# Kernel optimization log

Hardware: AMD Instinct MI355X
Metric: run time of the kernel (lower is better)

Reference implementation:

```python
import jax, jax.numpy as jnp
import numpy as np

H = 128          # hidden/context/decoder dim
HEADS = 4
HEAD_DIM = H // HEADS
MAX_LENGTH = 64
VOCAB = 3


def _lstm_step(h, c, x, Wih, Whh, b):
    # PyTorch gate order: i, f, g, o
    gates = x @ Wih.T + h @ Whh.T + b
    i, f, g, o = jnp.split(gates, 4, axis=-1)
    c = jax.nn.sigmoid(f) * c + jax.nn.sigmoid(i) * jnp.tanh(g)
    h = jax.nn.sigmoid(o) * jnp.tanh(c)
    return h, c


def _run_lstm(x, Wih, Whh, b):
    # x: (T, B, D) -> (T, B, H); zero initial state (PyTorch default)
    B = x.shape[1]
    Hh = Whh.shape[1]
    init = (jnp.zeros((B, Hh), x.dtype), jnp.zeros((B, Hh), x.dtype))
    def step(carry, xt):
        h, c = carry
        h, c = _lstm_step(h, c, xt, Wih, Whh, b)
        return (h, c), h
    _, ys = jax.lax.scan(step, init, x)
    return ys


def setup_inputs() -> dict:
    key = jax.random.key(0)
    T, B, D = 512, 64, 1024
    ks = jax.random.split(key, 20)
    def p(k, shape, s=0.05):
        return jax.random.normal(k, shape, dtype=jnp.float32) * s
    return {
        "cnn_output": p(ks[0], (T, B, D), 1.0),
        # encoder LSTM (2 layers); biases fused (b_ih + b_hh)
        "enc_Wih0": p(ks[1], (4 * H, D)),
        "enc_Whh0": p(ks[2], (4 * H, H)),
        "enc_b0": p(ks[3], (4 * H,)),
        "enc_Wih1": p(ks[4], (4 * H, H)),
        "enc_Whh1": p(ks[5], (4 * H, H)),
        "enc_b1": p(ks[6], (4 * H,)),
        # MultiheadAttention(embed_dim=128, num_heads=4)
        "attn_in_w": p(ks[7], (3 * H, H)),
        "attn_in_b": p(ks[8], (3 * H,)),
        "attn_out_w": p(ks[9], (H, H)),
        "attn_out_b": p(ks[10], (H,)),
        # decoder LSTM (2 layers), input dim 256
        "dec_Wih0": p(ks[11], (4 * H, 2 * H)),
        "dec_Whh0": p(ks[12], (4 * H, H)),
        "dec_b0": p(ks[13], (4 * H,)),
        "dec_Wih1": p(ks[14], (4 * H, H)),
        "dec_Whh1": p(ks[15], (4 * H, H)),
        "dec_b1": p(ks[16], (4 * H,)),
        # output projection
        "lin_w": p(ks[17], (VOCAB, H)),
        "lin_b": p(ks[18], (VOCAB,)),
    }


def reference(cnn_output, enc_Wih0, enc_Whh0, enc_b0, enc_Wih1, enc_Whh1, enc_b1,
              attn_in_w, attn_in_b, attn_out_w, attn_out_b,
              dec_Wih0, dec_Whh0, dec_b0, dec_Wih1, dec_Whh1, dec_b1,
              lin_w, lin_b):
    T, B, _ = cnn_output.shape
    # ---- encoder: 2-layer LSTM over T ----
    enc = _run_lstm(cnn_output, enc_Wih0, enc_Whh0, enc_b0)
    enc = _run_lstm(enc, enc_Wih1, enc_Whh1, enc_b1)          # (T, B, H)

    # ---- precompute attention keys/values (encoding is fixed) ----
    Wq, Wk, Wv = jnp.split(attn_in_w, 3, axis=0)
    bq, bk, bv = jnp.split(attn_in_b, 3, axis=0)
    K = (enc @ Wk.T + bk).reshape(T, B, HEADS, HEAD_DIM)      # (T,B,h,d)
    V = (enc @ Wv.T + bv).reshape(T, B, HEADS, HEAD_DIM)
    scale = 1.0 / np.sqrt(HEAD_DIM)

    # ---- 64-step attention + 2-layer LSTM decode loop ----
    out0 = jnp.zeros((B, H), cnn_output.dtype)
    h0 = jnp.zeros((2, B, H), cnn_output.dtype)
    c0 = jnp.zeros((2, B, H), cnn_output.dtype)

    def step(carry, _):
        out, h, c = carry
        q = ((out @ Wq.T + bq) * scale).reshape(B, HEADS, HEAD_DIM)
        scores = jnp.einsum("bhd,tbhd->bht", q, K)            # (B,h,T)
        attn = jax.nn.softmax(scores, axis=-1)
        ctx = jnp.einsum("bht,tbhd->bhd", attn, V).reshape(B, H)
        ctx = ctx @ attn_out_w.T + attn_out_b
        x = jnp.concatenate([out, ctx], axis=-1)              # (B, 2H)
        nh0, nc0 = _lstm_step(h[0], c[0], x, dec_Wih0, dec_Whh0, dec_b0)
        nh1, nc1 = _lstm_step(h[1], c[1], nh0, dec_Wih1, dec_Whh1, dec_b1)
        new_out = jax.nn.relu(nh1)
        y = new_out @ lin_w.T + lin_b                          # (B, vocab)
        return (new_out, jnp.stack([nh0, nh1]), jnp.stack([nc0, nc1])), y

    _, ys = jax.lax.scan(step, (out0, h0, c0), None, length=MAX_LENGTH)
    return ys                                                  # (64, B, vocab)
```

## Files before the change

### kernel.cpp

```cpp
#include <hip/hip_runtime.h>
#include <math.h>

#define T_LEN 512
#define BATCH 64
#define HID 128
#define G4 512

#define OFF_WQ2   0
#define OFF_WXO   16384
#define OFF_WXC   81920
#define OFF_WHH0b 147456
#define OFF_WIH1b 212992
#define OFF_WHH1b 278528
#define W2_TOTAL  344064

__device__ __forceinline__ float sigf(float x) { return 1.0f / (1.0f + __expf(-x)); }

__device__ __forceinline__ unsigned short f2bf(float x) {
    unsigned u = __float_as_uint(x);
    unsigned r = (u + 0x7fffu + ((u >> 16) & 1u)) >> 16;
    return (unsigned short)r;
}

__device__ __forceinline__ void cvt8(uint4 u, float f[8]) {
    f[0] = __uint_as_float(u.x << 16); f[1] = __uint_as_float(u.x & 0xffff0000u);
    f[2] = __uint_as_float(u.y << 16); f[3] = __uint_as_float(u.y & 0xffff0000u);
    f[4] = __uint_as_float(u.z << 16); f[5] = __uint_as_float(u.z & 0xffff0000u);
    f[6] = __uint_as_float(u.w << 16); f[7] = __uint_as_float(u.w & 0xffff0000u);
}

#define KEEP4(Vv) asm volatile("" : "+v"((Vv).x), "+v"((Vv).y), "+v"((Vv).z), "+v"((Vv).w))

__device__ __forceinline__ void cstore(float* p, float v) {
    __hip_atomic_store(p, v, __ATOMIC_RELAXED, __HIP_MEMORY_SCOPE_AGENT);
}
__device__ __forceinline__ float cload(float* p) {
    return __hip_atomic_load(p, __ATOMIC_RELAXED, __HIP_MEMORY_SCOPE_AGENT);
}

__global__ __launch_bounds__(256) void gemm_bias(
    const float* __restrict__ A, const float* __restrict__ W,
    const float* __restrict__ bias, float* __restrict__ C,
    int M, int N, int K)
{
    __shared__ __align__(16) float As[16][128];
    __shared__ __align__(16) float Ws[16][128];
    const int tid = threadIdx.x;
    const int m0 = blockIdx.y * 128;
    const int n0 = blockIdx.x * 128;
    const int tx = tid & 15, ty = tid >> 4;
    const int lrow = tid >> 1, lk = (tid & 1) * 8;
    float acc[8][8] = {};
    for (int k0 = 0; k0 < K; k0 += 16) {
        const float* Ap = A + (size_t)(m0 + lrow) * K + k0 + lk;
        const float* Wp = W + (size_t)(n0 + lrow) * K + k0 + lk;
        float4 a0 = *(const float4*)Ap;
        float4 a1 = *(const float4*)(Ap + 4);
        float4 w0 = *(const float4*)Wp;
        float4 w1 = *(const float4*)(Wp + 4);
        __syncthreads();
        As[lk+0][lrow]=a0.x; As[lk+1][lrow]=a0.y; As[lk+2][lrow]=a0.z; As[lk+3][lrow]=a0.w;
        As[lk+4][lrow]=a1.x; As[lk+5][lrow]=a1.y; As[lk+6][lrow]=a1.z; As[lk+7][lrow]=a1.w;
        Ws[lk+0][lrow]=w0.x; Ws[lk+1][lrow]=w0.y; Ws[lk+2][lrow]=w0.z; Ws[lk+3][lrow]=w0.w;
        Ws[lk+4][lrow]=w1.x; Ws[lk+5][lrow]=w1.y; Ws[lk+6][lrow]=w1.z; Ws[lk+7][lrow]=w1.w;
        __syncthreads();
        #pragma unroll
        for (int kk = 0; kk < 16; ++kk) {
            float4 av0 = *(const float4*)&As[kk][ty*8];
            float4 av1 = *(const float4*)&As[kk][ty*8+4];
            float4 wv0 = *(const float4*)&Ws[kk][tx*8];
            float4 wv1 = *(const float4*)&Ws[kk][tx*8+4];
            float av[8] = {av0.x,av0.y,av0.z,av0.w,av1.x,av1.y,av1.z,av1.w};
            float wv[8] = {wv0.x,wv0.y,wv0.z,wv0.w,wv1.x,wv1.y,wv1.z,wv1.w};
            #pragma unroll
            for (int i = 0; i < 8; ++i)
                #pragma unroll
                for (int j = 0; j < 8; ++j)
                    acc[i][j] = fmaf(av[i], wv[j], acc[i][j]);
        }
    }
    float bj[8];
    #pragma unroll
    for (int j = 0; j < 8; ++j) bj[j] = bias[n0 + tx*8 + j];
    #pragma unroll
    for (int i = 0; i < 8; ++i) {
        float* cp = C + (size_t)(m0 + ty*8 + i) * N + n0 + tx*8;
        *(float4*)cp     = make_float4(acc[i][0]+bj[0], acc[i][1]+bj[1], acc[i][2]+bj[2], acc[i][3]+bj[3]);
        *(float4*)(cp+4) = make_float4(acc[i][4]+bj[4], acc[i][5]+bj[5], acc[i][6]+bj[6], acc[i][7]+bj[7]);
    }
}

__global__ __launch_bounds__(512) void lstm_rec(
    const float* __restrict__ X,
    const float* __restrict__ Whh,
    float* __restrict__ Hout)
{
    const int b = blockIdx.x;
    const int r = threadIdx.x;
    __shared__ __align__(16) float h_s[HID];
    __shared__ float gate_s[G4];
    float w[HID];
    #pragma unroll
    for (int k = 0; k < HID; k += 4) {
        float4 v = *(const float4*)(Whh + (size_t)r * HID + k);
        w[k] = v.x; w[k+1] = v.y; w[k+2] = v.z; w[k+3] = v.w;
    }
    float c = 0.f;
    if (r < HID) h_s[r] = 0.f;
    __syncthreads();
    float xv = X[(size_t)b * G4 + r];
    for (int t = 0; t < T_LEN; ++t) {
        float xnext = 0.f;
        if (t + 1 < T_LEN) xnext = X[(size_t)((t + 1) * BATCH + b) * G4 + r];
        float a0 = xv, a1 = 0.f, a2 = 0.f, a3 = 0.f;
        const float4* h4 = (const float4*)h_s;
        #pragma unroll
        for (int k = 0; k < HID/4; ++k) {
            float4 hv = h4[k];
            a0 = fmaf(w[4*k+0], hv.x, a0);
            a1 = fmaf(w[4*k+1], hv.y, a1);
            a2 = fmaf(w[4*k+2], hv.z, a2);
            a3 = fmaf(w[4*k+3], hv.w, a3);
        }
        gate_s[r] = (a0 + a1) + (a2 + a3);
        __syncthreads();
        if (r < HID) {
            float gi = gate_s[r], gf = gate_s[HID+r], gg = gate_s[2*HID+r], go = gate_s[3*HID+r];
            c = sigf(gf) * c + sigf(gi) * tanhf(gg);
            float h = sigf(go) * tanhf(c);
            h_s[r] = h;
            Hout[(size_t)(t * BATCH + b) * HID + r] = h;
        }
        __syncthreads();
        xv = xnext;
    }
}

__global__ __launch_bounds__(256) void kv_pack(
    const float* __restrict__ KVf, unsigned short* __restrict__ Kb,
    unsigned short* __restrict__ Vt)
{
    const int b = blockIdx.x & 63, tc = blockIdx.x >> 6;
    const int t0 = tc * 128;
    __shared__ unsigned short tile[128][130];
    const int half = threadIdx.x >> 7;
    const int d = threadIdx.x & 127;
    for (int tt = 0; tt < 128; tt += 2) {
        int trow = tt + half;
        int t = t0 + trow;
        const float* src = KVf + ((size_t)t * BATCH + b) * 256;
        Kb[((size_t)b * T_LEN + t) * HID + d] = f2bf(src[d]);
        tile[trow][d] = f2bf(src[128 + d]);
    }
    __syncthreads();
    for (int dd = 0; dd < 128; dd += 2) {
        int drow = dd + half;
        int ts = threadIdx.x & 127;
        Vt[((size_t)b * HID + drow) * T_LEN + t0 + ts] = tile[ts][drow];
    }
}

__global__ __launch_bounds__(256) void pack2(
    const float* __restrict__ attn_in_w,
    const float* __restrict__ dWih0, const float* __restrict__ dWhh0,
    const float* __restrict__ dWih1, const float* __restrict__ dWhh1,
    unsigned short* __restrict__ Wb2)
{
    int i = blockIdx.x * 256 + threadIdx.x;
    if (i >= W2_TOTAL) return;
    if (i >= OFF_WXC && i < OFF_WHH0b) return;
    float v;
    if (i < OFF_WXO) v = attn_in_w[i];
    else if (i < OFF_WXC) {
        int j = i - OFF_WXO; v = dWih0[(size_t)(j >> 7) * 256 + (j & 127)];
    }
    else if (i < OFF_WIH1b) v = dWhh0[i - OFF_WHH0b];
    else if (i < OFF_WHH1b) v = dWih1[i - OFF_WIH1b];
    else                    v = dWhh1[i - OFF_WHH1b];
    Wb2[i] = f2bf(v);
}

__global__ __launch_bounds__(256) void fuse_wxc(
    const float* __restrict__ dWih0, const float* __restrict__ ow,
    unsigned short* __restrict__ Wb2)
{
    __shared__ float ow_s[128 * 128];
    for (int i = threadIdx.x; i < 16384; i += 256) ow_s[i] = ow[i];
    __syncthreads();
    const int r = blockIdx.x * 2 + (threadIdx.x >> 7);
    const int c = threadIdx.x & 127;
    const float* wr = dWih0 + (size_t)r * 256 + 128;
    float acc = 0.f;
    #pragma unroll 8
    for (int j = 0; j < 128; ++j) acc = fmaf(wr[j], ow_s[j * 128 + c], acc);
    Wb2[OFF_WXC + r * 128 + c] = f2bf(acc);
}

__global__ __launch_bounds__(128) void fuse_b0(
    const float* __restrict__ dWih0, const float* __restrict__ ob,
    const float* __restrict__ db0, float* __restrict__ b0p)
{
    int r = blockIdx.x * 128 + threadIdx.x;
    const float* wr = dWih0 + (size_t)r * 256 + 128;
    float acc = db0[r];
    #pragma unroll 8
    for (int j = 0; j < 128; ++j) acc = fmaf(wr[j], ob[j], acc);
    b0p[r] = acc;
}

__global__ __launch_bounds__(512, 2) void decoder7(
    const unsigned short* __restrict__ Kb, const unsigned short* __restrict__ Vt,
    const unsigned short* __restrict__ Wb2, const float* __restrict__ b0p,
    const float* __restrict__ attn_b, const float* __restrict__ b1,
    const float* __restrict__ lw, const float* __restrict__ lb,
    int* __restrict__ flags, float* __restrict__ exh0, float* __restrict__ exh1,
    float* __restrict__ Y)
{
    extern __shared__ __align__(16) char dyn[];
    char* Kl = dyn;
    const int wid = blockIdx.x;
    const int b = wid & 63;
    const int half64 = wid >> 6;
    const int dbase = half64 * 64;
    const int pbase = 64 - dbase;
    const int tid = threadIdx.x;
    int* myflag = flags + wid * 16;
    int* pflag  = flags + (wid ^ 64) * 16;
    float* exh0b = exh0 + b * 256;
    float* exh1b = exh1 + b * 256;

    __shared__ __align__(16) float x_s[384];
    __shared__ __align__(16) float x1_s[256];
    __shared__ __align__(16) float q_s[HID];
    __shared__ __align__(16) float sc[4 * T_LEN];
    __shared__ float red[512];
    __shared__ __align__(16) float ctxp[4][HID];
    __shared__ float g_s[256];
    __shared__ float hmax[4], hden[4];

    {
        const unsigned short* Ksrc = Kb + (size_t)b * T_LEN * HID;
        for (int c = tid; c < T_LEN * HID / 8; c += 512) {
            int t = c >> 4, k16 = c & 15;
            uint4 v = *(const uint4*)(Ksrc + c * 8);
            *(uint4*)(Kl + t * 256 + ((k16 * 16) ^ ((t & 15) << 4))) = v;
        }
    }
    const int lr = tid >> 1, halfk = tid & 1;
    const int r0 = (lr >> 6) * 128 + dbase + (lr & 63);
    uint4 W0[24], W1[16], WQ[4];
    #pragma unroll
    for (int i = 0; i < 24; ++i) {
        int ge = halfk * 192 + i * 8;
        const unsigned short* src =
            (ge < 128) ? Wb2 + OFF_WXO   + (size_t)r0 * HID + ge
          : (ge < 256) ? Wb2 + OFF_WXC   + (size_t)r0 * HID + (ge - 128)
                       : Wb2 + OFF_WHH0b + (size_t)r0 * HID + (ge - 256);
        W0[i] = *(const uint4*)src;
    }
    #pragma unroll
    for (int i = 0; i < 16; ++i) {
        int ge = halfk * 128 + i * 8;
        const unsigned short* src =
            (ge < 128) ? Wb2 + OFF_WIH1b + (size_t)r0 * HID + ge
                       : Wb2 + OFF_WHH1b + (size_t)r0 * HID + (ge - 128);
        W1[i] = *(const uint4*)src;
    }
    const int qrow = tid >> 2, qpart = tid & 3;
    #pragma unroll
    for (int i = 0; i < 4; ++i)
        WQ[i] = *(const uint4*)(Wb2 + OFF_WQ2 + (size_t)qrow * HID + qpart * 32 + i * 8);
    #pragma unroll
    for (int i = 0; i < 24; ++i) KEEP4(W0[i]);
    #pragma unroll
    for (int i = 0; i < 16; ++i) KEEP4(W1[i]);
    #pragma unroll
    for (int i = 0; i < 4; ++i) KEEP4(WQ[i]);

    const float b0r = b0p[r0];
    const float b1r = b1[r0];
    const float bqv = attn_b[qrow];
    float c0 = 0.f, c1 = 0.f;
    if (tid < 384) x_s[tid] = 0.f;
    if (tid < 256) x1_s[tid] = 0.f;
    __syncthreads();
    const float scale = 0.17677669529663687f;
    const int g = tid >> 7, l = tid & 127;

    for (int step = 0; step < 64; ++step) {
        #pragma unroll
        for (int i = 0; i < 24; ++i) KEEP4(W0[i]);
        #pragma unroll
        for (int i = 0; i < 16; ++i) KEEP4(W1[i]);
        #pragma unroll
        for (int i = 0; i < 4; ++i) KEEP4(WQ[i]);
        const int par = step & 1;
        if (step > 0) {
            if (tid == 0)
                while (__hip_atomic_load(pflag, __ATOMIC_RELAXED, __HIP_MEMORY_SCOPE_AGENT) < 2*step + 1)
                    __builtin_amdgcn_s_sleep(1);
            asm volatile("" ::: "memory");
            __syncthreads();
            if (tid < 64) {
                float hp = cload(&exh1b[((step - 1) & 1) * 128 + pbase + tid]);
                x1_s[128 + pbase + tid] = hp;
                x_s[pbase + tid] = fmaxf(hp, 0.f);
            }
            __syncthreads();
        }
        if (step > 0 && half64 == 0 && tid < 24) {
            const int row = tid >> 3, part = tid & 7;
            const float* wr = lw + row * HID + part * 16;
            const float* os = x_s + part * 16;
            float acc = 0.f;
            #pragma unroll
            for (int k = 0; k < 16; ++k) acc = fmaf(wr[k], os[k], acc);
            acc += __shfl_xor(acc, 1);
            acc += __shfl_xor(acc, 2);
            acc += __shfl_xor(acc, 4);
            if (part == 0) Y[((size_t)(step - 1) * BATCH + b) * 3 + row] = acc + lb[row];
        }
        {
            float acc = 0.f;
            const float* os = x_s + qpart * 32;
            #pragma unroll
            for (int i = 0; i < 4; ++i) {
                float f[8]; cvt8(WQ[i], f);
                const float* o8 = os + i * 8;
                acc += f[0]*o8[0]+f[1]*o8[1]+f[2]*o8[2]+f[3]*o8[3]
                     + f[4]*o8[4]+f[5]*o8[5]+f[6]*o8[6]+f[7]*o8[7];
            }
            acc += __shfl_xor(acc, 1);
            acc += __shfl_xor(acc, 2);
            if (qpart == 0) q_s[qrow] = (acc + bqv) * scale;
        }
        __syncthreads();
        {
            const int t = tid;
            float acc[4] = {0.f, 0.f, 0.f, 0.f};
            #pragma unroll
            for (int k16 = 0; k16 < 16; ++k16) {
                uint4 u = *(const uint4*)(Kl + t * 256 + ((k16 * 16) ^ ((t & 15) << 4)));
                float f[8]; cvt8(u, f);
                float4 q0 = *(const float4*)(q_s + k16 * 8);
                float4 q1 = *(const float4*)(q_s + k16 * 8 + 4);
                acc[k16 >> 2] += f[0]*q0.x + f[1]*q0.y + f[2]*q0.z + f[3]*q0.w
                               + f[4]*q1.x + f[5]*q1.y + f[6]*q1.z + f[7]*q1.w;
            }
            #pragma unroll
            for (int h = 0; h < 4; ++h) sc[h * T_LEN + t] = acc[h];
        }
        __syncthreads();
        float v[4];
        float mx = -3.4e38f;
        #pragma unroll
        for (int i = 0; i < 4; ++i) { v[i] = sc[g*T_LEN + l + 128*i]; mx = fmaxf(mx, v[i]); }
        red[tid] = mx;
        __syncthreads();
        if (l < 64) {
            float m2 = fmaxf(red[g*128 + l], red[g*128 + l + 64]);
            #pragma unroll
            for (int s = 32; s > 0; s >>= 1) m2 = fmaxf(m2, __shfl_xor(m2, s, 64));
            if (l == 0) hmax[g] = m2;
        }
        __syncthreads();
        float hm = hmax[g];
        float s4 = 0.f;
        #pragma unroll
        for (int i = 0; i < 4; ++i) {
            float e = __expf(v[i] - hm);
            sc[g*T_LEN + l + 128*i] = e;
            s4 += e;
        }
        red[tid] = s4;
        __syncthreads();
        if (l < 64) {
            float s2 = red[g*128 + l] + red[g*128 + l + 64];
            #pragma unroll
            for (int s = 32; s > 0; s >>= 1) s2 += __shfl_xor(s2, s, 64);
            if (l == 0) hden[g] = s2;
        }
        __syncthreads();
        {
            const int d = tid & 127, ch = tid >> 7;
            const unsigned short* vr = Vt + ((size_t)b * HID + d) * T_LEN + ch * 128;
            const float* scr = sc + (d >> 5) * T_LEN + ch * 128;
            float acc = 0.f;
            #pragma unroll
            for (int k = 0; k < 128; k += 8) {
                float f[8]; cvt8(*(const uint4*)(vr + k), f);
                #pragma unroll
                for (int j = 0; j < 8; ++j) acc = fmaf(f[j], scr[k + j], acc);
            }
            ctxp[ch][d] = acc;
        }
        __syncthreads();
        if (tid < HID)
            x_s[HID + tid] = (ctxp[0][tid] + ctxp[1][tid] + ctxp[2][tid] + ctxp[3][tid]) / hden[tid >> 5];
        __syncthreads();
        {
            float acc = 0.f;
            #pragma unroll
            for (int i = 0; i < 24; ++i) {
                float f[8]; cvt8(W0[i], f);
                const float* xp = x_s + halfk * 192 + i * 8;
                acc += f[0]*xp[0]+f[1]*xp[1]+f[2]*xp[2]+f[3]*xp[3]
                     + f[4]*xp[4]+f[5]*xp[5]+f[6]*xp[6]+f[7]*xp[7];
            }
            acc += __shfl_xor(acc, 1);
            if (halfk == 0) g_s[lr] = acc + b0r;
        }
        __syncthreads();
        if (tid < 64) {
            float gi = g_s[tid], gf = g_s[64+tid], gg = g_s[128+tid], go = g_s[192+tid];
            c0 = sigf(gf) * c0 + sigf(gi) * tanhf(gg);
            float h = sigf(go) * tanhf(c0);
            x_s[256 + dbase + tid] = h;
            x1_s[dbase + tid] = h;
            cstore(&exh0b[par * 128 + dbase + tid], h);
        }
        __syncthreads();
        if (tid == 0) {
            asm volatile("s_waitcnt vmcnt(0)" ::: "memory");
            __hip_atomic_store(myflag, 2*step + 2, __ATOMIC_RELEASE, __HIP_MEMORY_SCOPE_AGENT);
        }
        if (tid == 0)
            while (__hip_atomic_load(pflag, __ATOMIC_ACQUIRE, __HIP_MEMORY_SCOPE_AGENT) < 2*step + 2)
                __builtin_amdgcn_s_sleep(1);
        asm volatile("" ::: "memory");
        __syncthreads();
        if (tid < 64) {
            float hp = cload(&exh0b[par * 128 + pbase + tid]);
            x_s[256 + pbase + tid] = hp;
            x1_s[pbase + tid] = hp;
        }
        __syncthreads();
        {
            float acc = 0.f;
            #pragma unroll
            for (int i = 0; i < 16; ++i) {
                float f[8]; cvt8(W1[i], f);
                const float* xp = x1_s + halfk * 128 + i * 8;
                acc += f[0]*xp[0]+f[1]*xp[1]+f[2]*xp[2]+f[3]*xp[3]
                     + f[4]*xp[4]+f[5]*xp[5]+f[6]*xp[6]+f[7]*xp[7];
            }
            acc += __shfl_xor(acc, 1);
            if (halfk == 0) g_s[lr] = acc + b1r;
        }
        __syncthreads();
        if (tid < 64) {
            float gi = g_s[tid], gf = g_s[64+tid], gg = g_s[128+tid], go = g_s[192+tid];
            c1 = sigf(gf) * c1 + sigf(gi) * tanhf(gg);
            float h = sigf(go) * tanhf(c1);
            x1_s[128 + dbase + tid] = h;
            x_s[dbase + tid] = fmaxf(h, 0.f);
            cstore(&exh1b[par * 128 + dbase + tid], h);
        }
        __syncthreads();
        if (tid == 0) {
            asm volatile("s_waitcnt vmcnt(0)" ::: "memory");
            __hip_atomic_store(myflag, 2*step + 3, __ATOMIC_RELEASE, __HIP_MEMORY_SCOPE_AGENT);
        }
        __syncthreads();
    }
    if (tid == 0)
        while (__hip_atomic_load(pflag, __ATOMIC_ACQUIRE, __HIP_MEMORY_SCOPE_AGENT) < 129)
            __builtin_amdgcn_s_sleep(1);
    asm volatile("" ::: "memory");
    __syncthreads();
    if (tid < 64)
        x_s[pbase + tid] = fmaxf(cload(&exh1b[128 + pbase + tid]), 0.f);
    __syncthreads();
    if (half64 == 0 && tid < 24) {
        const int row = tid >> 3, part = tid & 7;
        const float* wr = lw + row * HID + part * 16;
        const float* os = x_s + part * 16;
        float acc = 0.f;
        #pragma unroll
        for (int k = 0; k < 16; ++k) acc = fmaf(wr[k], os[k], acc);
        acc += __shfl_xor(acc, 1);
        acc += __shfl_xor(acc, 2);
        acc += __shfl_xor(acc, 4);
        if (part == 0) Y[((size_t)63 * BATCH + b) * 3 + row] = acc + lb[row];
    }
}

extern "C" void kernel_launch(void* const* d_in, const int* in_sizes, int n_in,
                              void* d_out, int out_size, void* d_ws, size_t ws_size,
                              hipStream_t stream) {
    const float* cnn        = (const float*)d_in[0];
    const float* eWih0      = (const float*)d_in[1];
    const float* eWhh0      = (const float*)d_in[2];
    const float* eb0        = (const float*)d_in[3];
    const float* eWih1      = (const float*)d_in[4];
    const float* eWhh1      = (const float*)d_in[5];
    const float* eb1        = (const float*)d_in[6];
    const float* attn_in_w  = (const float*)d_in[7];
    const float* attn_in_b  = (const float*)d_in[8];
    const float* attn_out_w = (const float*)d_in[9];
    const float* attn_out_b = (const float*)d_in[10];
    const float* dWih0      = (const float*)d_in[11];
    const float* dWhh0      = (const float*)d_in[12];
    const float* db0        = (const float*)d_in[13];
    const float* dWih1      = (const float*)d_in[14];
    const float* dWhh1      = (const float*)d_in[15];
    const float* db1        = (const float*)d_in[16];
    const float* lin_w      = (const float*)d_in[17];
    const float* lin_b      = (const float*)d_in[18];
    float* Y  = (float*)d_out;

    float* ws = (float*)d_ws;
    float* X  = ws;
    float* Hb = X + (size_t)32768 * 512;
    unsigned short* Kb  = (unsigned short*)(Hb + (size_t)32768 * 128);
    unsigned short* Vt  = Kb + (size_t)BATCH * T_LEN * HID;
    unsigned short* Wb2 = Vt + (size_t)BATCH * HID * T_LEN;
    float* b0p  = (float*)(Wb2 + W2_TOTAL);
    int*   flags = (int*)(b0p + 512);
    float* exh0 = (float*)(flags + 128 * 16);
    float* exh1 = exh0 + 64 * 256;

    const int M = T_LEN * BATCH;

    (void)hipFuncSetAttribute((const void*)decoder7,
                              hipFuncAttributeMaxDynamicSharedMemorySize, 131072);

    (void)hipMemsetAsync(flags, 0, 128 * 16 * 4 + 2 * 64 * 256 * 4, stream);

    pack2<<<(W2_TOTAL + 255) / 256, 256, 0, stream>>>(attn_in_w, dWih0, dWhh0, dWih1, dWhh1, Wb2);
    fuse_wxc<<<256, 256, 0, stream>>>(dWih0, attn_out_w, Wb2);
    fuse_b0<<<4, 128, 0, stream>>>(dWih0, attn_out_b, db0, b0p);

    gemm_bias<<<dim3(4, M/128), 256, 0, stream>>>(cnn, eWih0, eb0, X, M, 512, 1024);
    lstm_rec<<<BATCH, 512, 0, stream>>>(X, eWhh0, Hb);
    gemm_bias<<<dim3(4, M/128), 256, 0, stream>>>(Hb, eWih1, eb1, X, M, 512, 128);
    lstm_rec<<<BATCH, 512, 0, stream>>>(X, eWhh1, Hb);
    gemm_bias<<<dim3(2, M/128), 256, 0, stream>>>(Hb, attn_in_w + 128*128, attn_in_b + 128,
                                                  X, M, 256, 128);
    kv_pack<<<256, 256, 0, stream>>>(X, Kb, Vt);
    decoder7<<<128, 512, 131072, stream>>>(Kb, Vt, Wb2, b0p,
                                           attn_in_b, db1, lin_w, lin_b,
                                           flags, exh0, exh1, Y);
}
```

Measured before the change: 2.964 ms.

## Use bf16 MFMA for encoder input GEMM and split LSTM recurrence across threads

Converts the CNN input and the first encoder input weight matrix to bf16 and runs the large input projection with an MFMA 16x16x32 bf16 kernel. Gate pre-activations are stored as bf16 to halve their traffic. The recurrent LSTM kernel now uses 1024 threads, with two threads per gate row reducing through a shuffle, and uses a fast exp-based tanh. This targets the FP32 FMA GEMM and the serial recurrence latency, at the cost of extra pack passes over a large input and lower precision in the gates.

```diff
diff --git a/kernel.cpp b/kernel.cpp
--- a/kernel.cpp
+++ b/kernel.cpp
@@ -14,12 +14,22 @@
 #define OFF_WHH1b 278528
 #define W2_TOTAL  344064
 
+typedef __attribute__((ext_vector_type(8))) short short8b;
+typedef __attribute__((ext_vector_type(4))) float f32x4;
+
 __device__ __forceinline__ float sigf(float x) { return 1.0f / (1.0f + __expf(-x)); }
+__device__ __forceinline__ float tanhfast(float x) {
+    float e = __expf(2.f * x);
+    return 1.f - 2.f / (e + 1.f);
+}
 
 __device__ __forceinline__ unsigned short f2bf(float x) {
     unsigned u = __float_as_uint(x);
     unsigned r = (u + 0x7fffu + ((u >> 16) & 1u)) >> 16;
     return (unsigned short)r;
+}
+__device__ __forceinline__ float bf2f(unsigned short u) {
+    return __uint_as_float((unsigned)u << 16);
 }
 
 __device__ __forceinline__ void cvt8(uint4 u, float f[8]) {
@@ -38,10 +48,92 @@
     return __hip_atomic_load(p, __ATOMIC_RELAXED, __HIP_MEMORY_SCOPE_AGENT);
 }
 
+__global__ __launch_bounds__(256) void pack_bf(
+    const float* __restrict__ src, unsigned short* __restrict__ dst, long n8)
+{
+    long i = (long)blockIdx.x * 256 + threadIdx.x;
+    long stride = (long)gridDim.x * 256;
+    for (; i < n8; i += stride) {
+        const float* s = src + i * 8;
+        float4 a = *(const float4*)s;
+        float4 b = *(const float4*)(s + 4);
+        uint4 o;
+        o.x = (unsigned)f2bf(a.x) | ((unsigned)f2bf(a.y) << 16);
+        o.y = (unsigned)f2bf(a.z) | ((unsigned)f2bf(a.w) << 16);
+        o.z = (unsigned)f2bf(b.x) | ((unsigned)f2bf(b.y) << 16);
+        o.w = (unsigned)f2bf(b.z) | ((unsigned)f2bf(b.w) << 16);
+        *(uint4*)(dst + i * 8) = o;
+    }
+}
+
+__global__ __launch_bounds__(256) void gemm_mfma_bf16(
+    const unsigned short* __restrict__ A, const unsigned short* __restrict__ B,
+    const float* __restrict__ bias, unsigned short* __restrict__ C,
+    int M, int N, int K)
+{
+    __shared__ __align__(16) unsigned char As[128 * 128];
+    __shared__ __align__(16) unsigned char Bs[128 * 128];
+    const int tid = threadIdx.x;
+    const int lane = tid & 63, wave = tid >> 6;
+    const int wr = wave >> 1, wc = wave & 1;
+    const int m0 = blockIdx.y * 128, n0 = blockIdx.x * 128;
+    f32x4 acc[4][4] = {};
+    const int lr = lane & 15, g = lane >> 4;
+
+    for (int k0 = 0; k0 < K; k0 += 64) {
+        __syncthreads();
+        #pragma unroll
+        for (int i = 0; i < 4; ++i) {
+            int c = tid + i * 256;
+            int row = c >> 3, cb = (c & 7) * 16;
+            int swz = cb ^ ((row & 7) << 4);
+            uint4 va = *(const uint4*)(A + (size_t)(m0 + row) * K + k0 + (c & 7) * 8);
+            *(uint4*)(As + row * 128 + swz) = va;
+            uint4 vb = *(const uint4*)(B + (size_t)(n0 + row) * K + k0 + (c & 7) * 8);
+            *(uint4*)(Bs + row * 128 + swz) = vb;
+        }
+        __syncthreads();
+        #pragma unroll
+        for (int kh = 0; kh < 2; ++kh) {
+            const int cb = kh * 64 + g * 16;
+            short8b af[4], bfr[4];
+            #pragma unroll
+            for (int m = 0; m < 4; ++m) {
+                int row = wr * 64 + m * 16 + lr;
+                af[m] = *(const short8b*)(As + row * 128 + (cb ^ ((row & 7) << 4)));
+            }
+            #pragma unroll
+            for (int n = 0; n < 4; ++n) {
+                int row = wc * 64 + n * 16 + lr;
+                bfr[n] = *(const short8b*)(Bs + row * 128 + (cb ^ ((row & 7) << 4)));
+            }
+            #pragma unroll
+            for (int m = 0; m < 4; ++m)
+                #pragma unroll
+                for (int n = 0; n < 4; ++n)
+                    acc[m][n] = __builtin_amdgcn_mfma_f32_16x16x32_bf16(
+                        af[m], bfr[n], acc[m][n], 0, 0, 0);
+        }
+    }
+    #pragma unroll
+    for (int n = 0; n < 4; ++n) {
+        int col = n0 + wc * 64 + n * 16 + lr;
+        float bv = bias[col];
+        #pragma unroll
+        for (int m = 0; m < 4; ++m) {
+            #pragma unroll
+            for (int j = 0; j < 4; ++j) {
+                int row = m0 + wr * 64 + m * 16 + g * 4 + j;
+                C[(size_t)row * N + col] = f2bf(acc[m][n][j] + bv);
+            }
+        }
+    }
+}
+
 __global__ __launch_bounds__(256) void gemm_bias(
     const float* __restrict__ A, const float* __restrict__ W,
-    const float* __restrict__ bias, float* __restrict__ C,
-    int M, int N, int K)
+    const float* __restrict__ bias, void* __restrict__ Cv,
+    int M, int N, int K, int bf16out)
 {
     __shared__ __align__(16) float As[16][128];
     __shared__ __align__(16) float Ws[16][128];
@@ -82,54 +174,72 @@
     float bj[8];
     #pragma unroll
     for (int j = 0; j < 8; ++j) bj[j] = bias[n0 + tx*8 + j];
-    #pragma unroll
-    for (int i = 0; i < 8; ++i) {
-        float* cp = C + (size_t)(m0 + ty*8 + i) * N + n0 + tx*8;
-        *(float4*)cp     = make_float4(acc[i][0]+bj[0], acc[i][1]+bj[1], acc[i][2]+bj[2], acc[i][3]+bj[3]);
-        *(float4*)(cp+4) = make_float4(acc[i][4]+bj[4], acc[i][5]+bj[5], acc[i][6]+bj[6], acc[i][7]+bj[7]);
-    }
-}
-
-__global__ __launch_bounds__(512) void lstm_rec(
-    const float* __restrict__ X,
+    if (bf16out) {
+        unsigned short* Ch = (unsigned short*)Cv;
+        #pragma unroll
+        for (int i = 0; i < 8; ++i) {
+            uint4 o;
+            o.x = (unsigned)f2bf(acc[i][0]+bj[0]) | ((unsigned)f2bf(acc[i][1]+bj[1]) << 16);
+            o.y = (unsigned)f2bf(acc[i][2]+bj[2]) | ((unsigned)f2bf(acc[i][3]+bj[3]) << 16);
+            o.z = (unsigned)f2bf(acc[i][4]+bj[4]) | ((unsigned)f2bf(acc[i][5]+bj[5]) << 16);
+            o.w = (unsigned)f2bf(acc[i][6]+bj[6]) | ((unsigned)f2bf(acc[i][7]+bj[7]) << 16);
+            *(uint4*)(Ch + (size_t)(m0 + ty*8 + i) * N + n0 + tx*8) = o;
+        }
+    } else {
+        float* Cf = (float*)Cv;
+        #pragma unroll
+        for (int i = 0; i < 8; ++i) {
+            float* cp = Cf + (size_t)(m0 + ty*8 + i) * N + n0 + tx*8;
+            *(float4*)cp     = make_float4(acc[i][0]+bj[0], acc[i][1]+bj[1], acc[i][2]+bj[2], acc[i][3]+bj[3]);
+            *(float4*)(cp+4) = make_float4(acc[i][4]+bj[4], acc[i][5]+bj[5], acc[i][6]+bj[6], acc[i][7]+bj[7]);
+        }
+    }
+}
+
+__global__ __launch_bounds__(1024) void lstm_rec2(
+    const unsigned short* __restrict__ X,
     const float* __restrict__ Whh,
     float* __restrict__ Hout)
 {
     const int b = blockIdx.x;
-    const int r = threadIdx.x;
+    const int tid = threadIdx.x;
+    const int r = tid >> 1, half = tid & 1;
     __shared__ __align__(16) float h_s[HID];
     __shared__ float gate_s[G4];
-    float w[HID];
-    #pragma unroll
-    for (int k = 0; k < HID; k += 4) {
-        float4 v = *(const float4*)(Whh + (size_t)r * HID + k);
-        w[k] = v.x; w[k+1] = v.y; w[k+2] = v.z; w[k+3] = v.w;
+    float4 w4[16];
+    {
+        const float4* wr4 = (const float4*)(Whh + (size_t)r * HID + half * 64);
+        #pragma unroll
+        for (int i = 0; i < 16; ++i) w4[i] = wr4[i];
     }
     float c = 0.f;
-    if (r < HID) h_s[r] = 0.f;
+    if (tid < HID) h_s[tid] = 0.f;
     __syncthreads();
-    float xv = X[(size_t)b * G4 + r];
+    float xv = (half == 0) ? bf2f(X[(size_t)b * G4 + r]) : 0.f;
     for (int t = 0; t < T_LEN; ++t) {
         float xnext = 0.f;
-        if (t + 1 < T_LEN) xnext = X[(size_t)((t + 1) * BATCH + b) * G4 + r];
-        float a0 = xv, a1 = 0.f, a2 = 0.f, a3 = 0.f;
-        const float4* h4 = (const float4*)h_s;
-        #pragma unroll
-        for (int k = 0; k < HID/4; ++k) {
+        if (half == 0 && t + 1 < T_LEN)
+            xnext = bf2f(X[(size_t)((t + 1) * BATCH + b) * G4 + r]);
+        float a0 = 0.f, a1 = 0.f, a2 = 0.f, a3 = 0.f;
+        const float4* h4 = (const float4*)(h_s + half * 64);
+        #pragma unroll
+        for (int k = 0; k < 16; ++k) {
             float4 hv = h4[k];
-            a0 = fmaf(w[4*k+0], hv.x, a0);
-            a1 = fmaf(w[4*k+1], hv.y, a1);
-            a2 = fmaf(w[4*k+2], hv.z, a2);
-            a3 = fmaf(w[4*k+3], hv.w, a3);
-        }
-        gate_s[r] = (a0 + a1) + (a2 + a3);
-        __syncthreads();
-        if (r < HID) {
-            float gi = gate_s[r], gf = gate_s[HID+r], gg = gate_s[2*HID+r], go = gate_s[3*HID+r];
-            c = sigf(gf) * c + sigf(gi) * tanhf(gg);
-            float h = sigf(go) * tanhf(c);
-            h_s[r] = h;
-            Hout[(size_t)(t * BATCH + b) * HID + r] = h;
+            a0 = fmaf(w4[k].x, hv.x, a0);
+            a1 = fmaf(w4[k].y, hv.y, a1);
+            a2 = fmaf(w4[k].z, hv.z, a2);
+            a3 = fmaf(w4[k].w, hv.w, a3);
+        }
+        float tot = (a0 + a1) + (a2 + a3);
+        tot += __shfl_xor(tot, 1);
+        if (half == 0) gate_s[r] = tot + xv;
+        __syncthreads();
+        if (tid < HID) {
+            float gi = gate_s[tid], gf = gate_s[HID+tid], gg = gate_s[2*HID+tid], go = gate_s[3*HID+tid];
+            c = sigf(gf) * c + sigf(gi) * tanhfast(gg);
+            float h = sigf(go) * tanhfast(c);
+            h_s[tid] = h;
+            Hout[(size_t)(t * BATCH + b) * HID + tid] = h;
         }
         __syncthreads();
         xv = xnext;
@@ -509,10 +619,15 @@
     const float* lin_b      = (const float*)d_in[18];
     float* Y  = (float*)d_out;
 
-    float* ws = (float*)d_ws;
-    float* X  = ws;
-    float* Hb = X + (size_t)32768 * 512;
-    unsigned short* Kb  = (unsigned short*)(Hb + (size_t)32768 * 128);
+    const int M = T_LEN * BATCH;
+
+    unsigned short* Xbf = (unsigned short*)d_ws;
+    float* Hb = (float*)(Xbf + (size_t)M * 512);
+    float* Creg = Hb + (size_t)M * 128;
+    unsigned short* cnn_bf = (unsigned short*)Creg;
+    unsigned short* wih0_bf = (unsigned short*)Hb;
+    float* KVf = Creg;
+    unsigned short* Kb  = (unsigned short*)(Creg + (size_t)M * 256);
     unsigned short* Vt  = Kb + (size_t)BATCH * T_LEN * HID;
     unsigned short* Wb2 = Vt + (size_t)BATCH * HID * T_LEN;
     float* b0p  = (float*)(Wb2 + W2_TOTAL);
@@ -520,24 +635,22 @@
     float* exh0 = (float*)(flags + 128 * 16);
     float* exh1 = exh0 + 64 * 256;
 
-    const int M = T_LEN * BATCH;
-
     (void)hipFuncSetAttribute((const void*)decoder7,
                               hipFuncAttributeMaxDynamicSharedMemorySize, 131072);
 
+    pack_bf<<<2048, 256, 0, stream>>>(cnn, cnn_bf, (long)M * 1024 / 8);
+    pack_bf<<<256, 256, 0, stream>>>(eWih0, wih0_bf, (long)512 * 1024 / 8);
+    gemm_mfma_bf16<<<dim3(4, M/128), 256, 0, stream>>>(cnn_bf, wih0_bf, eb0, Xbf, M, 512, 1024);
     (void)hipMemsetAsync(flags, 0, 128 * 16 * 4 + 2 * 64 * 256 * 4, stream);
-
     pack2<<<(W2_TOTAL + 255) / 256, 256, 0, stream>>>(attn_in_w, dWih0, dWhh0, dWih1, dWhh1, Wb2);
     fuse_wxc<<<256, 256, 0, stream>>>(dWih0, attn_out_w, Wb2);
     fuse_b0<<<4, 128, 0, stream>>>(dWih0, attn_out_b, db0, b0p);
-
-    gemm_bias<<<dim3(4, M/128), 256, 0, stream>>>(cnn, eWih0, eb0, X, M, 512, 1024);
-    lstm_rec<<<BATCH, 512, 0, stream>>>(X, eWhh0, Hb);
-    gemm_bias<<<dim3(4, M/128), 256, 0, stream>>>(Hb, eWih1, eb1, X, M, 512, 128);
-    lstm_rec<<<BATCH, 512, 0, stream>>>(X, eWhh1, Hb);
+    lstm_rec2<<<BATCH, 1024, 0, stream>>>(Xbf, eWhh0, Hb);
+    gemm_bias<<<dim3(4, M/128), 256, 0, stream>>>(Hb, eWih1, eb1, (void*)Xbf, M, 512, 128, 1);
+    lstm_rec2<<<BATCH, 1024, 0, stream>>>(Xbf, eWhh1, Hb);
     gemm_bias<<<dim3(2, M/128), 256, 0, stream>>>(Hb, attn_in_w + 128*128, attn_in_b + 128,
-                                                  X, M, 256, 128);
-    kv_pack<<<256, 256, 0, stream>>>(X, Kb, Vt);
+                                                  (void*)KVf, M, 256, 128, 0);
+    kv_pack<<<256, 256, 0, stream>>>(KVf, Kb, Vt);
     decoder7<<<128, 512, 131072, stream>>>(Kb, Vt, Wb2, b0p,
                                            attn_in_b, db1, lin_w, lin_b,
                                            flags, exh0, exh1, Y);
```

After: 2.685 ms. -9.4%, faster.
